# Optimization experiments

Measured on AMD Instinct MI355X. Metric: run time of the kernel, lower is better.

## Reference

```python
import jax, jax.numpy as jnp
import numpy as np

H = 16  # num_attention_heads


def setup_inputs() -> dict:
    key = jax.random.key(0)
    k1, k2, k3 = jax.random.split(key, 3)
    B, S, E = 2, 2048, 1024
    return {
        "hidden_states": jax.random.normal(k1, (B, S, E), dtype=jnp.float32),
        "W_attn": jax.random.normal(k2, (E, 3 * E), dtype=jnp.float32) * 0.02,
        "b_attn": jnp.zeros((3 * E,), dtype=jnp.float32),
        "W_proj": jax.random.normal(k3, (E, E), dtype=jnp.float32) * 0.02,
        "b_proj": jnp.zeros((E,), dtype=jnp.float32),
    }


def reference(hidden_states, W_attn, b_attn, W_proj, b_proj):
    B, S, E = hidden_states.shape
    hd = E // H
    # Conv1D: x @ W + b -> [B, S, 3E]
    qkv = hidden_states @ W_attn + b_attn
    # Faithful to module: _split_heads with 3*head_dim FIRST, then split q/k/v.
    # i.e. per-head slice of size 3*hd is [q_h | k_h | v_h] (interleaved layout).
    qkv = qkv.reshape(B, S, H, 3 * hd).transpose(0, 2, 1, 3)  # [B, H, S, 3*hd]
    q, k, v = jnp.split(qkv, 3, axis=-1)                      # each [B, H, S, hd]
    # scores, scaled by sqrt(head_dim) (value.size(-1) ** 0.5)
    scores = jnp.einsum("bhqd,bhkd->bhqk", q, k) / jnp.asarray(hd, q.dtype) ** 0.5
    # causal mask via where with masked_bias = -10000.0 (not -inf), as in module
    causal = jnp.tril(jnp.ones((S, S), dtype=bool))
    scores = jnp.where(causal, scores, jnp.asarray(-10000.0, scores.dtype))
    attn_weights = jax.nn.softmax(scores, axis=-1)  # dropout p=0 -> identity
    attn_out = jnp.einsum("bhqk,bhkd->bhqd", attn_weights, v)
    attn_out = attn_out.transpose(0, 2, 1, 3).reshape(B, S, E)  # merge heads
    return attn_out @ W_proj + b_proj
```

## Files before the change

### kernel.cpp

```cpp
#include <hip/hip_runtime.h>
#include <hip/hip_bf16.h>


typedef __attribute__((ext_vector_type(4))) float f32x4;
typedef __attribute__((ext_vector_type(16))) float f32x16;
typedef __attribute__((ext_vector_type(8))) short short8;
typedef __attribute__((ext_vector_type(2))) unsigned int uint2v;

#define AS1 __attribute__((address_space(1)))
#define AS3 __attribute__((address_space(3)))

__device__ __forceinline__ void load_lds16(const void* g, void* l) {
    __builtin_amdgcn_global_load_lds((const AS1 void*)g, (AS3 void*)l, 16, 0, 0);
}

__device__ __forceinline__ unsigned short f2bf(float f) {
    union { float f; unsigned int u; } v; v.f = f;
    unsigned int r = v.u + 0x7FFFu + ((v.u >> 16) & 1u);
    return (unsigned short)(r >> 16);
}

__device__ __forceinline__ int cvt_pk_bf16(float lo, float hi) {
    int r;
    asm("v_cvt_pk_bf16_f32 %0, %1, %2" : "=v"(r) : "v"(lo), "v"(hi));
    return r;
}

__device__ __forceinline__ float fexp2(float x) {
    float r;
    asm("v_exp_f32 %0, %1" : "=v"(r) : "v"(x));
    return r;
}

__device__ __forceinline__ void transpose_tile(
    const float* __restrict__ W, unsigned short* __restrict__ Wt,
    int K, int N, int bx, int by, int t) {
    __shared__ float tile[32][33];
    int k0 = by * 32, n0 = bx * 32;
    int r = t >> 3, c = (t & 7) * 4;
    float4 v = *(const float4*)&W[(size_t)(k0 + r) * N + n0 + c];
    tile[r][c] = v.x; tile[r][c + 1] = v.y; tile[r][c + 2] = v.z; tile[r][c + 3] = v.w;
    __syncthreads();
    int n = t >> 3; int kk = (t & 7) * 4;
    ushort4 o;
    o.x = f2bf(tile[kk + 0][n]);
    o.y = f2bf(tile[kk + 1][n]);
    o.z = f2bf(tile[kk + 2][n]);
    o.w = f2bf(tile[kk + 3][n]);
    *(ushort4*)&Wt[(size_t)(n0 + n) * K + k0 + kk] = o;
}

__global__ __launch_bounds__(256) void prep(
    const float* __restrict__ hs, unsigned short* __restrict__ Xb,
    const float* __restrict__ W_attn, unsigned short* __restrict__ WaT,
    const float* __restrict__ W_proj, unsigned short* __restrict__ WpT) {
    int bid = blockIdx.x, t = threadIdx.x;
    if (bid < 4096) {
        int i = (bid * 256 + t) * 4;
        float4 v = *(const float4*)(hs + i);
        ushort4 o;
        o.x = f2bf(v.x); o.y = f2bf(v.y); o.z = f2bf(v.z); o.w = f2bf(v.w);
        *(ushort4*)(Xb + i) = o;
    } else if (bid < 7168) {
        int r = bid - 4096;
        transpose_tile(W_attn, WaT, 1024, 3072, r % 96, r / 96, t);
    } else {
        int r = bid - 7168;
        transpose_tile(W_proj, WpT, 1024, 1024, r % 32, r / 32, t);
    }
}

__global__ __launch_bounds__(256) void gemm_qkv(
    const unsigned short* __restrict__ A,
    const unsigned short* __restrict__ Bt,
    const float* __restrict__ bias,
    unsigned short* __restrict__ qk, unsigned short* __restrict__ Vt,
    int M, int N, int K) {
    __shared__ unsigned short Sh[2][8192];
    unsigned short* Tb = &Sh[0][0];
    const int t = threadIdx.x, wave = t >> 6, lane = t & 63;
    const int l15 = lane & 15, quad = lane >> 4;
    const int m0 = blockIdx.y * 128, n0 = blockIdx.x * 128;
    const int srow = wave * 32 + (lane >> 2);
    const int sch = (lane & 3) * 8;
    const unsigned short* Ag = A + (size_t)(m0 + srow) * K + sch;
    const unsigned short* Bg = Bt + (size_t)(n0 + srow) * K + sch;
    const int wOff = wave * 1024;
    const int wm = (wave >> 1) * 64, wn = (wave & 1) * 64;
    f32x4 acc[4][4] = {};
    const int NSTEP = K / 32;
    load_lds16(Ag, &Sh[0][wOff]);
    load_lds16(Ag + (size_t)16 * K, &Sh[0][wOff + 512]);
    load_lds16(Bg, &Sh[0][4096 + wOff]);
    load_lds16(Bg + (size_t)16 * K, &Sh[0][4096 + wOff + 512]);
    for (int kt = 0; kt < NSTEP; ++kt) {
        const int cur = kt & 1;
        const unsigned short* As = &Sh[cur][0];
        const unsigned short* Bs = &Sh[cur][4096];
        __syncthreads();
        if (kt + 1 < NSTEP) {
            const int k1 = (kt + 1) * 32;
            unsigned short* An = &Sh[cur ^ 1][0];
            unsigned short* Bn = &Sh[cur ^ 1][4096];
            load_lds16(Ag + k1, An + wOff);
            load_lds16(Ag + k1 + (size_t)16 * K, An + wOff + 512);
            load_lds16(Bg + k1, Bn + wOff);
            load_lds16(Bg + k1 + (size_t)16 * K, Bn + wOff + 512);
        }
        short8 af[4], bf[4];
#pragma unroll
        for (int i = 0; i < 4; ++i) {
            af[i] = *(const short8*)&As[(wm + i * 16 + l15) * 32 + quad * 8];
            bf[i] = *(const short8*)&Bs[(wn + i * 16 + l15) * 32 + quad * 8];
        }
        __builtin_amdgcn_s_setprio(1);
#pragma unroll
        for (int mt = 0; mt < 4; ++mt)
#pragma unroll
            for (int nt = 0; nt < 4; ++nt)
                acc[mt][nt] = __builtin_amdgcn_mfma_f32_16x16x32_bf16(af[mt], bf[nt], acc[mt][nt], 0, 0, 0);
        __builtin_amdgcn_s_setprio(0);
    }
    __syncthreads();
    const int rem = n0 % 192;
#pragma unroll
    for (int mt = 0; mt < 4; ++mt) {
        int mrow = m0 + wm + mt * 16 + quad * 4;
#pragma unroll
        for (int nt = 0; nt < 4; ++nt) {
            int col = n0 + wn + nt * 16 + l15;
            float bv = bias[col];
            int h = col / 192;
            int j = col - h * 192;
            if (j < 128) {
                float sc = (j < 64) ? 0.18033688011f : 1.0f;
#pragma unroll
                for (int r = 0; r < 4; ++r)
                    qk[(size_t)(mrow + r) * 2048 + h * 128 + j] = f2bf((acc[mt][nt][r] + bv) * sc);
            } else {
                int d = j - 128;
                int s_local = wm + mt * 16 + quad * 4;
                ushort4 pk;
                pk.x = f2bf(acc[mt][nt][0] + bv);
                pk.y = f2bf(acc[mt][nt][1] + bv);
                pk.z = f2bf(acc[mt][nt][2] + bv);
                pk.w = f2bf(acc[mt][nt][3] + bv);
                *(ushort4*)&Tb[d * 136 + s_local] = pk;
            }
        }
    }
    if (rem != 0) {
        __syncthreads();
        int vhalf = (rem == 64) ? 1 : 0;
        int h = (n0 + vhalf * 64) / 192;
        int b = m0 >> 11;
        unsigned short* vbase = Vt + ((size_t)(b * 16 + h) * 64) * 2048 + (m0 & 2047);
        int drow = t >> 4, ch = (t & 15) * 8;
#pragma unroll
        for (int rr = 0; rr < 4; ++rr) {
            int d = rr * 16 + drow;
            *(uint4*)(vbase + (size_t)d * 2048 + ch) = *(const uint4*)&Tb[d * 136 + ch];
        }
    }
}

__global__ __launch_bounds__(256) void gemm_proj(
    const unsigned short* __restrict__ A,
    const unsigned short* __restrict__ Bt,
    const float* __restrict__ bias,
    float* __restrict__ C, int M, int N, int K) {
    __shared__ unsigned short Sh[2][6144];
    const int t = threadIdx.x, wave = t >> 6, lane = t & 63;
    const int l15 = lane & 15, quad = lane >> 4;
    const int m0 = blockIdx.y * 128, n0 = blockIdx.x * 64;
    const int srowA = wave * 32 + (lane >> 2);
    const int sch = (lane & 3) * 8;
    const unsigned short* Ag = A + (size_t)(m0 + srowA) * K + sch;
    const unsigned short* Bg = Bt + (size_t)(n0 + wave * 16 + (lane >> 2)) * K + sch;
    const int aOff = wave * 1024, bOff = wave * 512;
    const int wm = (wave >> 1) * 64, wn = (wave & 1) * 32;
    f32x4 acc[4][2] = {};
    const int NSTEP = K / 32;
    load_lds16(Ag, &Sh[0][aOff]);
    load_lds16(Ag + (size_t)16 * K, &Sh[0][aOff + 512]);
    load_lds16(Bg, &Sh[0][4096 + bOff]);
    for (int kt = 0; kt < NSTEP; ++kt) {
        const int cur = kt & 1;
        const unsigned short* As = &Sh[cur][0];
        const unsigned short* Bs = &Sh[cur][4096];
        __syncthreads();
        if (kt + 1 < NSTEP) {
            const int k1 = (kt + 1) * 32;
            load_lds16(Ag + k1, &Sh[cur ^ 1][aOff]);
            load_lds16(Ag + k1 + (size_t)16 * K, &Sh[cur ^ 1][aOff + 512]);
            load_lds16(Bg + k1, &Sh[cur ^ 1][4096 + bOff]);
        }
        short8 af[4], bf[2];
#pragma unroll
        for (int i = 0; i < 4; ++i)
            af[i] = *(const short8*)&As[(wm + i * 16 + l15) * 32 + quad * 8];
#pragma unroll
        for (int i = 0; i < 2; ++i)
            bf[i] = *(const short8*)&Bs[(wn + i * 16 + l15) * 32 + quad * 8];
        __builtin_amdgcn_s_setprio(1);
#pragma unroll
        for (int mt = 0; mt < 4; ++mt)
#pragma unroll
            for (int nt = 0; nt < 2; ++nt)
                acc[mt][nt] = __builtin_amdgcn_mfma_f32_16x16x32_bf16(af[mt], bf[nt], acc[mt][nt], 0, 0, 0);
        __builtin_amdgcn_s_setprio(0);
    }
#pragma unroll
    for (int mt = 0; mt < 4; ++mt) {
        int mrow = m0 + wm + mt * 16 + quad * 4;
#pragma unroll
        for (int nt = 0; nt < 2; ++nt) {
            int col = n0 + wn + nt * 16 + l15;
            float bv = bias[col];
#pragma unroll
            for (int r = 0; r < 4; ++r)
                C[(size_t)(mrow + r) * N + col] = acc[mt][nt][r] + bv;
        }
    }
}

__global__ __launch_bounds__(512, 4) void attn5(
    const unsigned short* __restrict__ qk,
    const unsigned short* __restrict__ Vt,
    unsigned short* __restrict__ out) {
    const int S = 2048;
    __shared__ unsigned short Sh[16384];
    const int t = threadIdx.x, wave = t >> 6, lane = t & 63;
    const int l31 = lane & 31, half = lane >> 5;
    const int g = wave >> 2, gw = wave & 3;
    const int bid = blockIdx.x;
    const int qt = (bid < 256) ? (15 - (bid >> 5)) : ((bid - 256) >> 5);
    const int bh = bid & 31;
    const int b = bh >> 4, h = bh & 15;
    const unsigned short* qkb = qk + (size_t)b * S * 2048 + h * 128;
    const unsigned short* vtb = Vt + (size_t)bh * 64 * 2048;

    const int q0 = qt * 128 + gw * 32;
    short8 qf[4];
#pragma unroll
    for (int km = 0; km < 4; ++km)
        qf[km] = *(const short8*)(qkb + (size_t)(q0 + l31) * 2048 + km * 16 + half * 8);

    f32x16 o[2] = {};
    float lrun = 0.f;

    const int srow = t >> 3, ch16 = t & 7;
    const int swz = srow * 64 + ((ch16 ^ (srow & 7)) * 8);
    const int KTP = qt + 1;

    uint4 kE = *(const uint4*)(qkb + (size_t)srow * 2048 + 64 + ch16 * 8);
    uint4 kO = *(const uint4*)(qkb + (size_t)(64 + srow) * 2048 + 64 + ch16 * 8);
    uint4 vE = *(const uint4*)(vtb + (size_t)srow * 2048 + ch16 * 8);
    uint4 vO = *(const uint4*)(vtb + (size_t)srow * 2048 + 64 + ch16 * 8);

    const int qmax = q0 + 31;
    const int ksw = l31 & 7;
    int chs[4];
#pragma unroll
    for (int km = 0; km < 4; ++km)
        chs[km] = ((km * 2 + half) ^ ksw) * 8;
    const int krow = l31 * 64;
    const unsigned short* Ksg = Sh + (g ? 4096 : 0);
    const unsigned short* Vsg = Sh + 8192 + (g ? 4096 : 0);

    for (int p = 0; p < KTP; ++p) {
        *(uint4*)&Sh[swz] = kE;
        *(uint4*)&Sh[4096 + swz] = kO;
        *(uint4*)&Sh[8192 + swz] = vE;
        *(uint4*)&Sh[12288 + swz] = vO;
        __syncthreads();
        if (p + 1 < KTP) {
            const int k2 = (2 * p + 2) * 64, k3 = k2 + 64;
            kE = *(const uint4*)(qkb + (size_t)(k2 + srow) * 2048 + 64 + ch16 * 8);
            kO = *(const uint4*)(qkb + (size_t)(k3 + srow) * 2048 + 64 + ch16 * 8);
            vE = *(const uint4*)(vtb + (size_t)srow * 2048 + k2 + ch16 * 8);
            vO = *(const uint4*)(vtb + (size_t)srow * 2048 + k3 + ch16 * 8);
        }
        const int kb = (2 * p + g) * 64;
        if (kb <= qmax) {
            f32x16 s[2] = {};
            __builtin_amdgcn_s_setprio(1);
#pragma unroll
            for (int nt = 0; nt < 2; ++nt)
#pragma unroll
                for (int km = 0; km < 4; ++km) {
                    short8 kf = *(const short8*)&Ksg[nt * 2048 + krow + chs[km]];
                    s[nt] = __builtin_amdgcn_mfma_f32_32x32x16_bf16(kf, qf[km], s[nt], 0, 0, 0);
                }
            __builtin_amdgcn_s_setprio(0);

            if (kb + 63 > q0) {
#pragma unroll
                for (int nt = 0; nt < 2; ++nt)
#pragma unroll
                    for (int r = 0; r < 16; ++r) {
                        int kg = kb + nt * 32 + (r & 3) + 8 * (r >> 2) + 4 * half;
                        if (kg > q0 + l31) s[nt][r] = -1e30f;
                    }
            }

            int gd[2][4][2];
            float a0 = 0.f;
#pragma unroll
            for (int nt = 0; nt < 2; ++nt)
#pragma unroll
                for (int gg = 0; gg < 4; ++gg) {
                    float e0 = fexp2(s[nt][4 * gg + 0]);
                    float e1 = fexp2(s[nt][4 * gg + 1]);
                    float e2 = fexp2(s[nt][4 * gg + 2]);
                    float e3 = fexp2(s[nt][4 * gg + 3]);
                    a0 += (e0 + e1) + (e2 + e3);
                    gd[nt][gg][0] = cvt_pk_bf16(e0, e1);
                    gd[nt][gg][1] = cvt_pk_bf16(e2, e3);
                }
            lrun += a0;

            short8 paf[4];
#pragma unroll
            for (int km = 0; km < 4; ++km) {
                const int nt = km >> 1, m = km & 1;
                uint2v w0 = __builtin_amdgcn_permlane32_swap(
                    (unsigned)gd[nt][2 * m][0], (unsigned)gd[nt][2 * m + 1][0], false, false);
                uint2v w1 = __builtin_amdgcn_permlane32_swap(
                    (unsigned)gd[nt][2 * m][1], (unsigned)gd[nt][2 * m + 1][1], false, false);
                int4 v = {(int)w0[0], (int)w1[0], (int)w0[1], (int)w1[1]};
                paf[km] = __builtin_bit_cast(short8, v);
            }

            __builtin_amdgcn_s_setprio(1);
#pragma unroll
            for (int nt2 = 0; nt2 < 2; ++nt2)
#pragma unroll
                for (int km = 0; km < 4; ++km) {
                    short8 vf = *(const short8*)&Vsg[nt2 * 2048 + krow + chs[km]];
                    o[nt2] = __builtin_amdgcn_mfma_f32_32x32x16_bf16(paf[km], vf, o[nt2], 0, 0, 0);
                }
            __builtin_amdgcn_s_setprio(0);
        }
        __syncthreads();
    }

    float* Lf = (float*)Sh;
    const int cidx = gw * 64 + lane;
    if (g == 1) {
        float* dst = Lf + cidx * 17;
#pragma unroll
        for (int r = 0; r < 16; ++r) dst[r] = o[0][r];
        dst[16] = lrun;
    }
    __syncthreads();
    float lsum = lrun;
    if (g == 0) {
        const float* src = Lf + cidx * 17;
#pragma unroll
        for (int r = 0; r < 16; ++r) o[0][r] += src[r];
        lsum += src[16];
    }
    __syncthreads();
    if (g == 1) {
        float* dst = Lf + cidx * 16;
#pragma unroll
        for (int r = 0; r < 16; ++r) dst[r] = o[1][r];
    }
    __syncthreads();
    if (g == 0) {
        const float* src = Lf + cidx * 16;
#pragma unroll
        for (int r = 0; r < 16; ++r) o[1][r] += src[r];
        float tot = lsum + __shfl_xor(lsum, 32);
        unsigned short* ob = out + (size_t)b * S * 1024 + h * 64;
#pragma unroll
        for (int r = 0; r < 16; ++r) {
            int ql = (r & 3) + 8 * (r >> 2) + 4 * half;
            float inv = 1.0f / __shfl(tot, ql);
            size_t row = (size_t)(q0 + ql) * 1024;
            ob[row + l31] = f2bf(o[0][r] * inv);
            ob[row + 32 + l31] = f2bf(o[1][r] * inv);
        }
    }
}

extern "C" void kernel_launch(void* const* d_in, const int* in_sizes, int n_in,
                              void* d_out, int out_size, void* d_ws, size_t ws_size,
                              hipStream_t stream) {
    const float* hs     = (const float*)d_in[0];
    const float* W_attn = (const float*)d_in[1];
    const float* b_attn = (const float*)d_in[2];
    const float* W_proj = (const float*)d_in[3];
    const float* b_proj = (const float*)d_in[4];
    float* out = (float*)d_out;

    const int B = 2, S = 2048, E = 1024;
    const int M = B * S;
    const int N3 = 3 * E;

    unsigned short* Xb  = (unsigned short*)d_ws;
    unsigned short* WaT = Xb + (size_t)M * E;
    unsigned short* WpT = WaT + (size_t)N3 * E;
    unsigned short* qkb = WpT + (size_t)E * E;
    unsigned short* Vt  = qkb + (size_t)M * 2048;
    unsigned short* ao  = Vt + (size_t)M * E;

    prep<<<dim3(8192), 256, 0, stream>>>(hs, Xb, W_attn, WaT, W_proj, WpT);

    gemm_qkv<<<dim3(N3 / 128, M / 128), 256, 0, stream>>>(Xb, WaT, b_attn, qkb, Vt, M, N3, E);

    attn5<<<dim3(512), 512, 0, stream>>>(qkb, Vt, ao);

    gemm_proj<<<dim3(E / 64, M / 128), 256, 0, stream>>>(ao, WpT, b_proj, out, M, E, E);
}
```

Baseline: 168.1 us.

## Use 8 waves per block in QKV and projection GEMMs with split load roles

Both GEMM kernels move from 256 to 512 threads per block while keeping the same output tile. Each wave now computes a smaller sub-tile (2x4 or 2x2 MFMA tiles instead of 4x4 or 4x2), and waves are split so the first four stage A tiles and the last four stage B tiles into LDS. The aim is more waves per CU to hide LDS and global latency and to cut per-wave register pressure. The trade-off is more synchronisation participants and less MFMA work per LDS fragment load, so reuse per wave drops.

```diff
diff --git a/kernel.cpp b/kernel.cpp
--- a/kernel.cpp
+++ b/kernel.cpp
@@ -70,7 +70,7 @@
     }
 }
 
-__global__ __launch_bounds__(256) void gemm_qkv(
+__global__ __launch_bounds__(512, 6) void gemm_qkv(
     const unsigned short* __restrict__ A,
     const unsigned short* __restrict__ Bt,
     const float* __restrict__ bias,
@@ -81,18 +81,18 @@
     const int t = threadIdx.x, wave = t >> 6, lane = t & 63;
     const int l15 = lane & 15, quad = lane >> 4;
     const int m0 = blockIdx.y * 128, n0 = blockIdx.x * 128;
-    const int srow = wave * 32 + (lane >> 2);
+    const int sw = wave & 3;
+    const bool isB = wave >= 4;
+    const int srow = sw * 32 + (lane >> 2);
     const int sch = (lane & 3) * 8;
-    const unsigned short* Ag = A + (size_t)(m0 + srow) * K + sch;
-    const unsigned short* Bg = Bt + (size_t)(n0 + srow) * K + sch;
-    const int wOff = wave * 1024;
-    const int wm = (wave >> 1) * 64, wn = (wave & 1) * 64;
-    f32x4 acc[4][4] = {};
+    const unsigned short* G0 = isB ? (Bt + (size_t)(n0 + srow) * K + sch)
+                                   : (A + (size_t)(m0 + srow) * K + sch);
+    const int stOff = (isB ? 4096 : 0) + sw * 1024;
+    const int wr = wave >> 1, wc = wave & 1;
+    f32x4 acc[2][4] = {};
     const int NSTEP = K / 32;
-    load_lds16(Ag, &Sh[0][wOff]);
-    load_lds16(Ag + (size_t)16 * K, &Sh[0][wOff + 512]);
-    load_lds16(Bg, &Sh[0][4096 + wOff]);
-    load_lds16(Bg + (size_t)16 * K, &Sh[0][4096 + wOff + 512]);
+    load_lds16(G0, &Sh[0][stOff]);
+    load_lds16(G0 + (size_t)16 * K, &Sh[0][stOff + 512]);
     for (int kt = 0; kt < NSTEP; ++kt) {
         const int cur = kt & 1;
         const unsigned short* As = &Sh[cur][0];
@@ -100,22 +100,19 @@
         __syncthreads();
         if (kt + 1 < NSTEP) {
             const int k1 = (kt + 1) * 32;
-            unsigned short* An = &Sh[cur ^ 1][0];
-            unsigned short* Bn = &Sh[cur ^ 1][4096];
-            load_lds16(Ag + k1, An + wOff);
-            load_lds16(Ag + k1 + (size_t)16 * K, An + wOff + 512);
-            load_lds16(Bg + k1, Bn + wOff);
-            load_lds16(Bg + k1 + (size_t)16 * K, Bn + wOff + 512);
-        }
-        short8 af[4], bf[4];
-#pragma unroll
-        for (int i = 0; i < 4; ++i) {
-            af[i] = *(const short8*)&As[(wm + i * 16 + l15) * 32 + quad * 8];
-            bf[i] = *(const short8*)&Bs[(wn + i * 16 + l15) * 32 + quad * 8];
-        }
+            load_lds16(G0 + k1, &Sh[cur ^ 1][stOff]);
+            load_lds16(G0 + k1 + (size_t)16 * K, &Sh[cur ^ 1][stOff + 512]);
+        }
+        short8 af[2], bf[4];
+#pragma unroll
+        for (int i = 0; i < 2; ++i)
+            af[i] = *(const short8*)&As[(wr * 32 + i * 16 + l15) * 32 + quad * 8];
+#pragma unroll
+        for (int i = 0; i < 4; ++i)
+            bf[i] = *(const short8*)&Bs[(wc * 64 + i * 16 + l15) * 32 + quad * 8];
         __builtin_amdgcn_s_setprio(1);
 #pragma unroll
-        for (int mt = 0; mt < 4; ++mt)
+        for (int mt = 0; mt < 2; ++mt)
 #pragma unroll
             for (int nt = 0; nt < 4; ++nt)
                 acc[mt][nt] = __builtin_amdgcn_mfma_f32_16x16x32_bf16(af[mt], bf[nt], acc[mt][nt], 0, 0, 0);
@@ -124,11 +121,11 @@
     __syncthreads();
     const int rem = n0 % 192;
 #pragma unroll
-    for (int mt = 0; mt < 4; ++mt) {
-        int mrow = m0 + wm + mt * 16 + quad * 4;
+    for (int mt = 0; mt < 2; ++mt) {
+        int mrow = m0 + wr * 32 + mt * 16 + quad * 4;
 #pragma unroll
         for (int nt = 0; nt < 4; ++nt) {
-            int col = n0 + wn + nt * 16 + l15;
+            int col = n0 + wc * 64 + nt * 16 + l15;
             float bv = bias[col];
             int h = col / 192;
             int j = col - h * 192;
@@ -139,7 +136,7 @@
                     qk[(size_t)(mrow + r) * 2048 + h * 128 + j] = f2bf((acc[mt][nt][r] + bv) * sc);
             } else {
                 int d = j - 128;
-                int s_local = wm + mt * 16 + quad * 4;
+                int s_local = wr * 32 + mt * 16 + quad * 4;
                 ushort4 pk;
                 pk.x = f2bf(acc[mt][nt][0] + bv);
                 pk.y = f2bf(acc[mt][nt][1] + bv);
@@ -157,14 +154,14 @@
         unsigned short* vbase = Vt + ((size_t)(b * 16 + h) * 64) * 2048 + (m0 & 2047);
         int drow = t >> 4, ch = (t & 15) * 8;
 #pragma unroll
-        for (int rr = 0; rr < 4; ++rr) {
-            int d = rr * 16 + drow;
+        for (int rr = 0; rr < 2; ++rr) {
+            int d = rr * 32 + drow;
             *(uint4*)(vbase + (size_t)d * 2048 + ch) = *(const uint4*)&Tb[d * 136 + ch];
         }
     }
 }
 
-__global__ __launch_bounds__(256) void gemm_proj(
+__global__ __launch_bounds__(512, 4) void gemm_proj(
     const unsigned short* __restrict__ A,
     const unsigned short* __restrict__ Bt,
     const float* __restrict__ bias,
@@ -173,17 +170,18 @@
     const int t = threadIdx.x, wave = t >> 6, lane = t & 63;
     const int l15 = lane & 15, quad = lane >> 4;
     const int m0 = blockIdx.y * 128, n0 = blockIdx.x * 64;
-    const int srowA = wave * 32 + (lane >> 2);
+    const int sw = wave & 3;
+    const bool isB = wave >= 4;
+    const int srow = isB ? (sw * 16 + (lane >> 2)) : (sw * 32 + (lane >> 2));
     const int sch = (lane & 3) * 8;
-    const unsigned short* Ag = A + (size_t)(m0 + srowA) * K + sch;
-    const unsigned short* Bg = Bt + (size_t)(n0 + wave * 16 + (lane >> 2)) * K + sch;
-    const int aOff = wave * 1024, bOff = wave * 512;
-    const int wm = (wave >> 1) * 64, wn = (wave & 1) * 32;
-    f32x4 acc[4][2] = {};
+    const unsigned short* G0 = isB ? (Bt + (size_t)(n0 + srow) * K + sch)
+                                   : (A + (size_t)(m0 + srow) * K + sch);
+    const int stOff = isB ? (4096 + sw * 512) : (sw * 1024);
+    const int wr = wave >> 1, wc = wave & 1;
+    f32x4 acc[2][2] = {};
     const int NSTEP = K / 32;
-    load_lds16(Ag, &Sh[0][aOff]);
-    load_lds16(Ag + (size_t)16 * K, &Sh[0][aOff + 512]);
-    load_lds16(Bg, &Sh[0][4096 + bOff]);
+    load_lds16(G0, &Sh[0][stOff]);
+    if (!isB) load_lds16(G0 + (size_t)16 * K, &Sh[0][stOff + 512]);
     for (int kt = 0; kt < NSTEP; ++kt) {
         const int cur = kt & 1;
         const unsigned short* As = &Sh[cur][0];
@@ -191,31 +189,30 @@
         __syncthreads();
         if (kt + 1 < NSTEP) {
             const int k1 = (kt + 1) * 32;
-            load_lds16(Ag + k1, &Sh[cur ^ 1][aOff]);
-            load_lds16(Ag + k1 + (size_t)16 * K, &Sh[cur ^ 1][aOff + 512]);
-            load_lds16(Bg + k1, &Sh[cur ^ 1][4096 + bOff]);
-        }
-        short8 af[4], bf[2];
-#pragma unroll
-        for (int i = 0; i < 4; ++i)
-            af[i] = *(const short8*)&As[(wm + i * 16 + l15) * 32 + quad * 8];
+            load_lds16(G0 + k1, &Sh[cur ^ 1][stOff]);
+            if (!isB) load_lds16(G0 + k1 + (size_t)16 * K, &Sh[cur ^ 1][stOff + 512]);
+        }
+        short8 af[2], bf[2];
 #pragma unroll
         for (int i = 0; i < 2; ++i)
-            bf[i] = *(const short8*)&Bs[(wn + i * 16 + l15) * 32 + quad * 8];
+            af[i] = *(const short8*)&As[(wr * 32 + i * 16 + l15) * 32 + quad * 8];
+#pragma unroll
+        for (int i = 0; i < 2; ++i)
+            bf[i] = *(const short8*)&Bs[(wc * 32 + i * 16 + l15) * 32 + quad * 8];
         __builtin_amdgcn_s_setprio(1);
 #pragma unroll
-        for (int mt = 0; mt < 4; ++mt)
+        for (int mt = 0; mt < 2; ++mt)
 #pragma unroll
             for (int nt = 0; nt < 2; ++nt)
                 acc[mt][nt] = __builtin_amdgcn_mfma_f32_16x16x32_bf16(af[mt], bf[nt], acc[mt][nt], 0, 0, 0);
         __builtin_amdgcn_s_setprio(0);
     }
 #pragma unroll
-    for (int mt = 0; mt < 4; ++mt) {
-        int mrow = m0 + wm + mt * 16 + quad * 4;
+    for (int mt = 0; mt < 2; ++mt) {
+        int mrow = m0 + wr * 32 + mt * 16 + quad * 4;
 #pragma unroll
         for (int nt = 0; nt < 2; ++nt) {
-            int col = n0 + wn + nt * 16 + l15;
+            int col = n0 + wc * 32 + nt * 16 + l15;
             float bv = bias[col];
 #pragma unroll
             for (int r = 0; r < 4; ++r)
@@ -408,9 +405,9 @@
 
     prep<<<dim3(8192), 256, 0, stream>>>(hs, Xb, W_attn, WaT, W_proj, WpT);
 
-    gemm_qkv<<<dim3(N3 / 128, M / 128), 256, 0, stream>>>(Xb, WaT, b_attn, qkb, Vt, M, N3, E);
+    gemm_qkv<<<dim3(N3 / 128, M / 128), 512, 0, stream>>>(Xb, WaT, b_attn, qkb, Vt, M, N3, E);
 
     attn5<<<dim3(512), 512, 0, stream>>>(qkb, Vt, ao);
 
-    gemm_proj<<<dim3(E / 64, M / 128), 256, 0, stream>>>(ao, WpT, b_proj, out, M, E, E);
-}
+    gemm_proj<<<dim3(E / 64, M / 128), 512, 0, stream>>>(ao, WpT, b_proj, out, M, E, E);
+}
```

Measured after the change: 167.2 us. No clear change (-0.5%).

## Triple-buffer GEMM LDS pipelines and move attention K/V loads to async global_load_lds

Applied to the files above, without the earlier changes.

Both GEMM kernels go from double to triple LDS buffering with a prefetch distance of two. Explicit vmcnt waits plus a raw s_barrier replace __syncthreads, so one stage of loads stays in flight across the barrier. The attention kernel drops the register staging of K/V tiles and uses direct global-to-LDS loads into a double-buffered LDS region, with one barrier per iteration instead of two. This doubles attention LDS usage and adds 50% to GEMM LDS, which may lower occupancy. It also relies on hand-counted vmcnt values being correct.

```diff
diff --git a/kernel.cpp b/kernel.cpp
--- a/kernel.cpp
+++ b/kernel.cpp
@@ -76,7 +76,7 @@
     const float* __restrict__ bias,
     unsigned short* __restrict__ qk, unsigned short* __restrict__ Vt,
     int M, int N, int K) {
-    __shared__ unsigned short Sh[2][8192];
+    __shared__ unsigned short Sh[3][8192];
     unsigned short* Tb = &Sh[0][0];
     const int t = threadIdx.x, wave = t >> 6, lane = t & 63;
     const int l15 = lane & 15, quad = lane >> 4;
@@ -89,24 +89,32 @@
     const int wm = (wave >> 1) * 64, wn = (wave & 1) * 64;
     f32x4 acc[4][4] = {};
     const int NSTEP = K / 32;
-    load_lds16(Ag, &Sh[0][wOff]);
-    load_lds16(Ag + (size_t)16 * K, &Sh[0][wOff + 512]);
-    load_lds16(Bg, &Sh[0][4096 + wOff]);
-    load_lds16(Bg + (size_t)16 * K, &Sh[0][4096 + wOff + 512]);
+#pragma unroll
+    for (int pb = 0; pb < 2; ++pb) {
+        const int kk = pb * 32;
+        load_lds16(Ag + kk, &Sh[pb][wOff]);
+        load_lds16(Ag + kk + (size_t)16 * K, &Sh[pb][wOff + 512]);
+        load_lds16(Bg + kk, &Sh[pb][4096 + wOff]);
+        load_lds16(Bg + kk + (size_t)16 * K, &Sh[pb][4096 + wOff + 512]);
+    }
+    int cur = 0, stg = 2;
     for (int kt = 0; kt < NSTEP; ++kt) {
-        const int cur = kt & 1;
+        if (kt + 1 < NSTEP)
+            asm volatile("s_waitcnt vmcnt(4) lgkmcnt(0)" ::: "memory");
+        else
+            asm volatile("s_waitcnt vmcnt(0) lgkmcnt(0)" ::: "memory");
+        __builtin_amdgcn_s_barrier();
+        __builtin_amdgcn_sched_barrier(0);
+        if (kt + 2 < NSTEP) {
+            const int k2 = (kt + 2) * 32;
+            unsigned short* nb = &Sh[stg][0];
+            load_lds16(Ag + k2, nb + wOff);
+            load_lds16(Ag + k2 + (size_t)16 * K, nb + wOff + 512);
+            load_lds16(Bg + k2, nb + 4096 + wOff);
+            load_lds16(Bg + k2 + (size_t)16 * K, nb + 4096 + wOff + 512);
+        }
         const unsigned short* As = &Sh[cur][0];
         const unsigned short* Bs = &Sh[cur][4096];
-        __syncthreads();
-        if (kt + 1 < NSTEP) {
-            const int k1 = (kt + 1) * 32;
-            unsigned short* An = &Sh[cur ^ 1][0];
-            unsigned short* Bn = &Sh[cur ^ 1][4096];
-            load_lds16(Ag + k1, An + wOff);
-            load_lds16(Ag + k1 + (size_t)16 * K, An + wOff + 512);
-            load_lds16(Bg + k1, Bn + wOff);
-            load_lds16(Bg + k1 + (size_t)16 * K, Bn + wOff + 512);
-        }
         short8 af[4], bf[4];
 #pragma unroll
         for (int i = 0; i < 4; ++i) {
@@ -120,6 +128,8 @@
             for (int nt = 0; nt < 4; ++nt)
                 acc[mt][nt] = __builtin_amdgcn_mfma_f32_16x16x32_bf16(af[mt], bf[nt], acc[mt][nt], 0, 0, 0);
         __builtin_amdgcn_s_setprio(0);
+        cur = (cur == 2) ? 0 : cur + 1;
+        stg = (stg == 2) ? 0 : stg + 1;
     }
     __syncthreads();
     const int rem = n0 % 192;
@@ -169,7 +179,7 @@
     const unsigned short* __restrict__ Bt,
     const float* __restrict__ bias,
     float* __restrict__ C, int M, int N, int K) {
-    __shared__ unsigned short Sh[2][6144];
+    __shared__ unsigned short Sh[3][6144];
     const int t = threadIdx.x, wave = t >> 6, lane = t & 63;
     const int l15 = lane & 15, quad = lane >> 4;
     const int m0 = blockIdx.y * 128, n0 = blockIdx.x * 64;
@@ -181,20 +191,29 @@
     const int wm = (wave >> 1) * 64, wn = (wave & 1) * 32;
     f32x4 acc[4][2] = {};
     const int NSTEP = K / 32;
-    load_lds16(Ag, &Sh[0][aOff]);
-    load_lds16(Ag + (size_t)16 * K, &Sh[0][aOff + 512]);
-    load_lds16(Bg, &Sh[0][4096 + bOff]);
+#pragma unroll
+    for (int pb = 0; pb < 2; ++pb) {
+        const int kk = pb * 32;
+        load_lds16(Ag + kk, &Sh[pb][aOff]);
+        load_lds16(Ag + kk + (size_t)16 * K, &Sh[pb][aOff + 512]);
+        load_lds16(Bg + kk, &Sh[pb][4096 + bOff]);
+    }
+    int cur = 0, stg = 2;
     for (int kt = 0; kt < NSTEP; ++kt) {
-        const int cur = kt & 1;
+        if (kt + 1 < NSTEP)
+            asm volatile("s_waitcnt vmcnt(3) lgkmcnt(0)" ::: "memory");
+        else
+            asm volatile("s_waitcnt vmcnt(0) lgkmcnt(0)" ::: "memory");
+        __builtin_amdgcn_s_barrier();
+        __builtin_amdgcn_sched_barrier(0);
+        if (kt + 2 < NSTEP) {
+            const int k2 = (kt + 2) * 32;
+            load_lds16(Ag + k2, &Sh[stg][aOff]);
+            load_lds16(Ag + k2 + (size_t)16 * K, &Sh[stg][aOff + 512]);
+            load_lds16(Bg + k2, &Sh[stg][4096 + bOff]);
+        }
         const unsigned short* As = &Sh[cur][0];
         const unsigned short* Bs = &Sh[cur][4096];
-        __syncthreads();
-        if (kt + 1 < NSTEP) {
-            const int k1 = (kt + 1) * 32;
-            load_lds16(Ag + k1, &Sh[cur ^ 1][aOff]);
-            load_lds16(Ag + k1 + (size_t)16 * K, &Sh[cur ^ 1][aOff + 512]);
-            load_lds16(Bg + k1, &Sh[cur ^ 1][4096 + bOff]);
-        }
         short8 af[4], bf[2];
 #pragma unroll
         for (int i = 0; i < 4; ++i)
@@ -209,6 +228,8 @@
             for (int nt = 0; nt < 2; ++nt)
                 acc[mt][nt] = __builtin_amdgcn_mfma_f32_16x16x32_bf16(af[mt], bf[nt], acc[mt][nt], 0, 0, 0);
         __builtin_amdgcn_s_setprio(0);
+        cur = (cur == 2) ? 0 : cur + 1;
+        stg = (stg == 2) ? 0 : stg + 1;
     }
 #pragma unroll
     for (int mt = 0; mt < 4; ++mt) {
@@ -224,12 +245,12 @@
     }
 }
 
-__global__ __launch_bounds__(512, 4) void attn5(
+__global__ __launch_bounds__(512, 4) void attn6(
     const unsigned short* __restrict__ qk,
     const unsigned short* __restrict__ Vt,
     unsigned short* __restrict__ out) {
     const int S = 2048;
-    __shared__ unsigned short Sh[16384];
+    __shared__ unsigned short Sh[2][16384];
     const int t = threadIdx.x, wave = t >> 6, lane = t & 63;
     const int l31 = lane & 31, half = lane >> 5;
     const int g = wave >> 2, gw = wave & 3;
@@ -249,14 +270,17 @@
     f32x16 o[2] = {};
     float lrun = 0.f;
 
-    const int srow = t >> 3, ch16 = t & 7;
-    const int swz = srow * 64 + ((ch16 ^ (srow & 7)) * 8);
+    const int srow = t >> 3, c8 = t & 7;
+    const int gsw = ((c8 ^ (srow & 7)) * 8);
+    const int ldst = wave * 512;
+    const unsigned short* kSrc = qkb + (size_t)srow * 2048 + 64 + gsw;
+    const unsigned short* vSrc = vtb + (size_t)srow * 2048 + gsw;
     const int KTP = qt + 1;
 
-    uint4 kE = *(const uint4*)(qkb + (size_t)srow * 2048 + 64 + ch16 * 8);
-    uint4 kO = *(const uint4*)(qkb + (size_t)(64 + srow) * 2048 + 64 + ch16 * 8);
-    uint4 vE = *(const uint4*)(vtb + (size_t)srow * 2048 + ch16 * 8);
-    uint4 vO = *(const uint4*)(vtb + (size_t)srow * 2048 + 64 + ch16 * 8);
+    load_lds16(kSrc, &Sh[0][ldst]);
+    load_lds16(kSrc + (size_t)64 * 2048, &Sh[0][4096 + ldst]);
+    load_lds16(vSrc, &Sh[0][8192 + ldst]);
+    load_lds16(vSrc + 64, &Sh[0][12288 + ldst]);
 
     const int qmax = q0 + 31;
     const int ksw = l31 & 7;
@@ -265,87 +289,87 @@
     for (int km = 0; km < 4; ++km)
         chs[km] = ((km * 2 + half) ^ ksw) * 8;
     const int krow = l31 * 64;
-    const unsigned short* Ksg = Sh + (g ? 4096 : 0);
-    const unsigned short* Vsg = Sh + 8192 + (g ? 4096 : 0);
+    const int gOff = g ? 4096 : 0;
 
     for (int p = 0; p < KTP; ++p) {
-        *(uint4*)&Sh[swz] = kE;
-        *(uint4*)&Sh[4096 + swz] = kO;
-        *(uint4*)&Sh[8192 + swz] = vE;
-        *(uint4*)&Sh[12288 + swz] = vO;
+        const int cur = p & 1;
         __syncthreads();
         if (p + 1 < KTP) {
-            const int k2 = (2 * p + 2) * 64, k3 = k2 + 64;
-            kE = *(const uint4*)(qkb + (size_t)(k2 + srow) * 2048 + 64 + ch16 * 8);
-            kO = *(const uint4*)(qkb + (size_t)(k3 + srow) * 2048 + 64 + ch16 * 8);
-            vE = *(const uint4*)(vtb + (size_t)srow * 2048 + k2 + ch16 * 8);
-            vO = *(const uint4*)(vtb + (size_t)srow * 2048 + k3 + ch16 * 8);
+            const int k2 = (2 * p + 2) * 64;
+            unsigned short* nb = &Sh[cur ^ 1][0];
+            load_lds16(kSrc + (size_t)k2 * 2048, nb + ldst);
+            load_lds16(kSrc + (size_t)(k2 + 64) * 2048, nb + 4096 + ldst);
+            load_lds16(vSrc + k2, nb + 8192 + ldst);
+            load_lds16(vSrc + k2 + 64, nb + 12288 + ldst);
         }
         const int kb = (2 * p + g) * 64;
-        if (kb <= qmax) {
-            f32x16 s[2] = {};
-            __builtin_amdgcn_s_setprio(1);
+        if (kb > qmax) continue;
+
+        const unsigned short* Ksg = &Sh[cur][gOff];
+        const unsigned short* Vsg = &Sh[cur][8192 + gOff];
+
+        f32x16 s[2] = {};
+        __builtin_amdgcn_s_setprio(1);
+#pragma unroll
+        for (int nt = 0; nt < 2; ++nt)
+#pragma unroll
+            for (int km = 0; km < 4; ++km) {
+                short8 kf = *(const short8*)&Ksg[nt * 2048 + krow + chs[km]];
+                s[nt] = __builtin_amdgcn_mfma_f32_32x32x16_bf16(kf, qf[km], s[nt], 0, 0, 0);
+            }
+        __builtin_amdgcn_s_setprio(0);
+
+        if (kb + 63 > q0) {
 #pragma unroll
             for (int nt = 0; nt < 2; ++nt)
 #pragma unroll
-                for (int km = 0; km < 4; ++km) {
-                    short8 kf = *(const short8*)&Ksg[nt * 2048 + krow + chs[km]];
-                    s[nt] = __builtin_amdgcn_mfma_f32_32x32x16_bf16(kf, qf[km], s[nt], 0, 0, 0);
+                for (int r = 0; r < 16; ++r) {
+                    int kg = kb + nt * 32 + (r & 3) + 8 * (r >> 2) + 4 * half;
+                    if (kg > q0 + l31) s[nt][r] = -1e30f;
                 }
-            __builtin_amdgcn_s_setprio(0);
-
-            if (kb + 63 > q0) {
-#pragma unroll
-                for (int nt = 0; nt < 2; ++nt)
-#pragma unroll
-                    for (int r = 0; r < 16; ++r) {
-                        int kg = kb + nt * 32 + (r & 3) + 8 * (r >> 2) + 4 * half;
-                        if (kg > q0 + l31) s[nt][r] = -1e30f;
-                    }
+        }
+
+        int gd[2][4][2];
+        float a0 = 0.f;
+#pragma unroll
+        for (int nt = 0; nt < 2; ++nt)
+#pragma unroll
+            for (int gg = 0; gg < 4; ++gg) {
+                float e0 = fexp2(s[nt][4 * gg + 0]);
+                float e1 = fexp2(s[nt][4 * gg + 1]);
+                float e2 = fexp2(s[nt][4 * gg + 2]);
+                float e3 = fexp2(s[nt][4 * gg + 3]);
+                a0 += (e0 + e1) + (e2 + e3);
+                gd[nt][gg][0] = cvt_pk_bf16(e0, e1);
+                gd[nt][gg][1] = cvt_pk_bf16(e2, e3);
             }
-
-            int gd[2][4][2];
-            float a0 = 0.f;
-#pragma unroll
-            for (int nt = 0; nt < 2; ++nt)
-#pragma unroll
-                for (int gg = 0; gg < 4; ++gg) {
-                    float e0 = fexp2(s[nt][4 * gg + 0]);
-                    float e1 = fexp2(s[nt][4 * gg + 1]);
-                    float e2 = fexp2(s[nt][4 * gg + 2]);
-                    float e3 = fexp2(s[nt][4 * gg + 3]);
-                    a0 += (e0 + e1) + (e2 + e3);
-                    gd[nt][gg][0] = cvt_pk_bf16(e0, e1);
-                    gd[nt][gg][1] = cvt_pk_bf16(e2, e3);
-                }
-            lrun += a0;
-
-            short8 paf[4];
+        lrun += a0;
+
+        short8 paf[4];
+#pragma unroll
+        for (int km = 0; km < 4; ++km) {
+            const int nt = km >> 1, m = km & 1;
+            uint2v w0 = __builtin_amdgcn_permlane32_swap(
+                (unsigned)gd[nt][2 * m][0], (unsigned)gd[nt][2 * m + 1][0], false, false);
+            uint2v w1 = __builtin_amdgcn_permlane32_swap(
+                (unsigned)gd[nt][2 * m][1], (unsigned)gd[nt][2 * m + 1][1], false, false);
+            int4 v = {(int)w0[0], (int)w1[0], (int)w0[1], (int)w1[1]};
+            paf[km] = __builtin_bit_cast(short8, v);
+        }
+
+        __builtin_amdgcn_s_setprio(1);
+#pragma unroll
+        for (int nt2 = 0; nt2 < 2; ++nt2)
 #pragma unroll
             for (int km = 0; km < 4; ++km) {
-                const int nt = km >> 1, m = km & 1;
-                uint2v w0 = __builtin_amdgcn_permlane32_swap(
-                    (unsigned)gd[nt][2 * m][0], (unsigned)gd[nt][2 * m + 1][0], false, false);
-                uint2v w1 = __builtin_amdgcn_permlane32_swap(
-                    (unsigned)gd[nt][2 * m][1], (unsigned)gd[nt][2 * m + 1][1], false, false);
-                int4 v = {(int)w0[0], (int)w1[0], (int)w0[1], (int)w1[1]};
-                paf[km] = __builtin_bit_cast(short8, v);
+                short8 vf = *(const short8*)&Vsg[nt2 * 2048 + krow + chs[km]];
+                o[nt2] = __builtin_amdgcn_mfma_f32_32x32x16_bf16(paf[km], vf, o[nt2], 0, 0, 0);
             }
-
-            __builtin_amdgcn_s_setprio(1);
-#pragma unroll
-            for (int nt2 = 0; nt2 < 2; ++nt2)
-#pragma unroll
-                for (int km = 0; km < 4; ++km) {
-                    short8 vf = *(const short8*)&Vsg[nt2 * 2048 + krow + chs[km]];
-                    o[nt2] = __builtin_amdgcn_mfma_f32_32x32x16_bf16(paf[km], vf, o[nt2], 0, 0, 0);
-                }
-            __builtin_amdgcn_s_setprio(0);
-        }
-        __syncthreads();
-    }
-
-    float* Lf = (float*)Sh;
+        __builtin_amdgcn_s_setprio(0);
+    }
+    __syncthreads();
+
+    float* Lf = (float*)&Sh[0][0];
     const int cidx = gw * 64 + lane;
     if (g == 1) {
         float* dst = Lf + cidx * 17;
@@ -410,7 +434,7 @@
 
     gemm_qkv<<<dim3(N3 / 128, M / 128), 256, 0, stream>>>(Xb, WaT, b_attn, qkb, Vt, M, N3, E);
 
-    attn5<<<dim3(512), 512, 0, stream>>>(qkb, Vt, ao);
+    attn6<<<dim3(512), 512, 0, stream>>>(qkb, Vt, ao);
 
     gemm_proj<<<dim3(E / 64, M / 128), 256, 0, stream>>>(ao, WpT, b_proj, out, M, E, E);
 }
```

New measurement: 167.4 us. About the same (-0.4%).
